# Kernel optimization log

Measured on AMD Instinct MI355X. Metric: run time of the kernel, lower is better.

## Reference

```python
import jax, jax.numpy as jnp
import numpy as np

B, CIN, COUT, H, W = 4, 128, 128, 128, 128
K, G, PAD = 3, 4, 1  # kernel_size, deformable_groups, padding=(K-1)//2
CG = CIN // G


def setup_inputs() -> dict:
    key = jax.random.key(0)
    k1, k2, k3, k4 = jax.random.split(key, 4)
    x = jax.random.normal(k1, (B, CIN, H, W), jnp.float32)
    # 1x1 offset conv (in module it is zero-initialized; use small random values
    # so the bilinear-sampling path is actually exercised)
    w_off = jax.random.normal(k2, (G * K * K * 2, CIN), jnp.float32) * 0.01
    b_off = jax.random.normal(k3, (G * K * K * 2,), jnp.float32) * 0.1
    # DeformConv weight [Cout, Cin, K, K] (DCNv1 has no bias)
    w_def = jax.random.normal(k4, (COUT, CIN, K, K), jnp.float32) * (1.0 / np.sqrt(CIN * K * K))
    return {"x": x, "w_off": w_off, "b_off": b_off, "w_def": w_def}


def _deform_conv(x, offset, w):
    """DCNv1: per-location bilinear gather at offset positions, then weighted sum.

    x:      [B, CIN, H, W]
    offset: [B, G*K*K*2, H, W], channel layout (g, kk, {dy,dx})
    w:      [COUT, CIN, K, K]
    """
    off = offset.reshape(B, G, K * K, 2, H, W)
    ky, kx = np.meshgrid(np.arange(K), np.arange(K), indexing='ij')
    ky = jnp.asarray(ky.reshape(-1), jnp.float32)
    kx = jnp.asarray(kx.reshape(-1), jnp.float32)
    # sampling positions: p = p0 + p_k - pad + offset   -> [B, G, K*K, H, W]
    py = off[:, :, :, 0] + (ky - PAD).reshape(1, 1, K * K, 1, 1) \
         + jnp.arange(H, dtype=jnp.float32).reshape(1, 1, 1, H, 1)
    px = off[:, :, :, 1] + (kx - PAD).reshape(1, 1, K * K, 1, 1) \
         + jnp.arange(W, dtype=jnp.float32).reshape(1, 1, 1, 1, W)

    y0 = jnp.floor(py)
    x0 = jnp.floor(px)
    wy1 = py - y0
    wx1 = px - x0
    wy0 = 1.0 - wy1
    wx0 = 1.0 - wx1
    y0i = y0.astype(jnp.int32)
    x0i = x0.astype(jnp.int32)

    xg = x.reshape(B, G, CG, H * W)  # grouped channels for gather

    def gather(yi, xi):
        # zero padding outside the feature map (mmcv DeformConv semantics)
        valid = (yi >= 0) & (yi < H) & (xi >= 0) & (xi < W)
        idx = (jnp.clip(yi, 0, H - 1) * W + jnp.clip(xi, 0, W - 1)).reshape(B, G, 1, K * K * H * W)
        v = jnp.take_along_axis(xg, idx, axis=3).reshape(B, G, CG, K * K, H, W)
        return v * valid[:, :, None].astype(x.dtype)

    # accumulate the four bilinear corners sequentially to bound peak memory
    val = gather(y0i, x0i) * (wy0 * wx0)[:, :, None]
    val = val + gather(y0i, x0i + 1) * (wy0 * wx1)[:, :, None]
    val = val + gather(y0i + 1, x0i) * (wy1 * wx0)[:, :, None]
    val = val + gather(y0i + 1, x0i + 1) * (wy1 * wx1)[:, :, None]

    wg = w.reshape(COUT, G, CG, K * K)
    return jnp.einsum('bgckhw,ogck->bohw', val, wg)


def reference(x, w_off, b_off, w_def):
    # 1x1 offset conv with bias
    offset = jnp.einsum('bchw,oc->bohw', x, w_off) + b_off[None, :, None, None]
    return jax.nn.relu(_deform_conv(x, offset, w_def))
```

## Files before the change

kernel.cpp:

```cpp
#include <hip/hip_runtime.h>
#include <hip/hip_fp16.h>


#define HW 16384

typedef _Float16 h2 __attribute__((ext_vector_type(2)));
typedef _Float16 h8 __attribute__((ext_vector_type(8)));
typedef float floatx4 __attribute__((ext_vector_type(4)));

static __device__ __forceinline__ unsigned pkrtz(float a, float b) {
  auto h = __builtin_amdgcn_cvt_pkrtz(a, b);
  return __builtin_bit_cast(unsigned, h);
}
static __device__ __forceinline__ h2 u2h2(unsigned u) { return __builtin_bit_cast(h2, u); }
static __device__ __forceinline__ unsigned h2u(h2 h) { return __builtin_bit_cast(unsigned, h); }
static __device__ __forceinline__ h2 splat_lo(unsigned u) {
  unsigned v = (u & 0xffffu) | (u << 16); return u2h2(v);
}
static __device__ __forceinline__ h2 splat_hi(unsigned u) {
  unsigned v = (u >> 16) | (u & 0xffff0000u); return u2h2(v);
}

__global__ __launch_bounds__(256) void prep_w(
    const float* __restrict__ w_off, const float* __restrict__ w_def,
    _Float16* __restrict__ woff, _Float16* __restrict__ wdef) {
  int idx = blockIdx.x * 256 + threadIdx.x;
  int stride = gridDim.x * 256;
  for (int i = idx; i < 147456; i += stride) {
    int j = i & 7, l = (i >> 3) & 63, ot = (i >> 9) & 7, ks = (i >> 12) & 3, kk = i >> 14;
    int o = ot * 16 + (l & 15);
    int c = ks * 32 + ((l >> 4) << 3) + j;
    wdef[i] = (_Float16)w_def[(o * 128 + c) * 9 + kk];
  }
  for (int i = idx; i < 10240; i += stride) {
    int j = i & 7, l = (i >> 3) & 63, t = i >> 9;
    int mt = t % 5, ks = t / 5;
    int o = mt * 16 + (l & 15);
    int c = ks * 32 + ((l >> 4) << 3) + j;
    woff[i] = (o < 72) ? (_Float16)w_off[o * 128 + c] : (_Float16)0.f;
  }
}

__global__ __launch_bounds__(256) void prep_row(
    const float* __restrict__ x, const _Float16* __restrict__ woff,
    const float* __restrict__ b_off, unsigned* __restrict__ offs2,
    _Float16* __restrict__ x16) {
  __shared__ uint2 xpk[32 * 64];
  int tid = threadIdx.x, lane = tid & 63, wv = tid >> 6;
  int i = blockIdx.x;
  int L = (i & 7) * 128 + (i >> 3);
  int half = L & 1, h = (L >> 1) & 127, b = L >> 8;
  int p0 = half * 64;

#pragma unroll
  for (int it = 0; it < 2; it++) {
    int u = it * 256 + tid;
    int px4 = u & 15, cqq = u >> 4;
    const float* xp = x + (((size_t)b * 128 + cqq * 4) * 128 + h) * 128 + p0 + px4 * 4;
    float4 v0 = *(const float4*)xp;
    float4 v1 = *(const float4*)(xp + HW);
    float4 v2 = *(const float4*)(xp + 2 * HW);
    float4 v3 = *(const float4*)(xp + 3 * HW);
    uint2* dst = &xpk[cqq * 64 + px4 * 4];
    uint2 w;
    w.x = pkrtz(v0.x, v1.x); w.y = pkrtz(v2.x, v3.x); dst[0] = w;
    w.x = pkrtz(v0.y, v1.y); w.y = pkrtz(v2.y, v3.y); dst[1] = w;
    w.x = pkrtz(v0.z, v1.z); w.y = pkrtz(v2.z, v3.z); dst[2] = w;
    w.x = pkrtz(v0.w, v1.w); w.y = pkrtz(v2.w, v3.w); dst[3] = w;
  }
  __syncthreads();

  uint4* xrow = (uint4*)(x16 + (((size_t)b * 128 + h) * 128 + p0) * 128);
#pragma unroll
  for (int it = 0; it < 4; it++) {
    int u = it * 256 + tid;
    int oct = u & 15, px = u >> 4;
    uint2 a = xpk[(2 * oct) * 64 + px];
    uint2 c = xpk[(2 * oct + 1) * 64 + px];
    uint4 qv; qv.x = a.x; qv.y = a.y; qv.z = c.x; qv.w = c.y;
    xrow[px * 16 + oct] = qv;
  }

  floatx4 acc[5];
#pragma unroll
  for (int mt = 0; mt < 5; mt++) acc[mt] = (floatx4)0.f;
  const h8* A = (const h8*)woff;
  int q = lane >> 4, col = lane & 15;
  int pxl = wv * 16 + col;
#pragma unroll
  for (int ks = 0; ks < 4; ks++) {
    uint2 lo = xpk[(ks * 8 + 2 * q) * 64 + pxl];
    uint2 hi = xpk[(ks * 8 + 2 * q + 1) * 64 + pxl];
    uint4 qq; qq.x = lo.x; qq.y = lo.y; qq.z = hi.x; qq.w = hi.y;
    h8 bv = __builtin_bit_cast(h8, qq);
#pragma unroll
    for (int mt = 0; mt < 5; mt++)
      acc[mt] = __builtin_amdgcn_mfma_f32_16x16x32_f16(A[(ks * 5 + mt) * 64 + lane], bv, acc[mt], 0, 0, 0);
  }
#pragma unroll
  for (int mt = 0; mt < 5; mt++) {
    if (mt == 4 && q >= 2) continue;
    int o0 = mt * 16 + q * 4;
    float4 bo = *(const float4*)(b_off + o0);
    floatx4 f = acc[mt];
    unsigned* dst = offs2 + ((size_t)b * 36 + (o0 >> 1)) * HW + h * 128 + p0 + pxl;
    dst[0]  = pkrtz(f[0] + bo.x, f[1] + bo.y);
    dst[HW] = pkrtz(f[2] + bo.z, f[3] + bo.w);
  }
}

__global__ __launch_bounds__(256, 3) void deform_conv(
    const _Float16* __restrict__ x16, const _Float16* __restrict__ wdef,
    const unsigned* __restrict__ offs2, float* __restrict__ out) {
  __shared__ uint4 xs[5 * 128 * 5];

  int tid = threadIdx.x, lane = tid & 63, wv = tid >> 6;
  int i = blockIdx.x;
  int L = (i & 7) * 64 + (i >> 3);
  int b = L >> 7, h = L & 127;
  int rlo = min(max(h - 2, 0), 123);
  int pa = 32 * wv + (lane & 15);
  int q = lane >> 4;

  floatx4 acc[2][8];
#pragma unroll
  for (int f = 0; f < 2; f++)
#pragma unroll
    for (int ot = 0; ot < 8; ot++) acc[f][ot] = (floatx4)0.f;

  for (int t = 0; t < 4; t++) {
    __syncthreads();
    unsigned dd[9][2];
#pragma unroll
    for (int kk = 0; kk < 9; kk++)
#pragma unroll
      for (int f = 0; f < 2; f++)
        dd[kk][f] = offs2[((size_t)b * 36 + t * 9 + kk) * HW + h * 128 + pa + 16 * f];
#pragma unroll
    for (int it = 0; it < 10; it++) {
      int u = tid + it * 256;
      int oct = u & 3, v2 = u >> 2;
      int px = v2 & 127, r = v2 >> 7;
      const uint4* src = (const uint4*)(x16 + (((size_t)b * 128 + rlo + r) * 128 + px) * 128 + t * 32) + oct;
      xs[(r * 128 + px) * 5 + oct] = *src;
    }
    __syncthreads();

#pragma unroll
    for (int kk = 0; kk < 9; kk++) {
      const uint4* Ak = (const uint4*)wdef + (size_t)(kk * 2048 + t * 512);
      h8 av[8];
#pragma unroll
      for (int ot = 0; ot < 8; ot++) av[ot] = __builtin_bit_cast(h8, Ak[ot * 64 + lane]);
#pragma unroll
      for (int f = 0; f < 2; f++) {
        int p = pa + 16 * f;
        h2 d = u2h2(dd[kk][f]);
        float dy = (float)d[0], dx = (float)d[1];
        float py = (float)h + (float)(kk / 3 - 1) + dy;
        float pxs = (float)p + (float)(kk % 3 - 1) + dx;
        float y0f = floorf(py), x0f = floorf(pxs);
        int y0 = (int)y0f, x0 = (int)x0f;
        float wy1f = py - y0f, wx1 = pxs - x0f;
        float wy0f = 1.f - wy1f, wx0 = 1.f - wx1;
        int x1 = x0 + 1, y1 = y0 + 1;
        int xb = min(max(x0, 0), 126);
        float fx0 = (x0 >= 0 && x0 <= 127) ? 1.f : 0.f;
        float fx1 = (x1 >= 0 && x1 <= 127) ? 1.f : 0.f;
        float wAf = (x0 == xb ? wx0 * fx0 : 0.f) + (x1 == xb ? wx1 * fx1 : 0.f);
        float wBf = (x0 == xb + 1 ? wx0 * fx0 : 0.f) + (x1 == xb + 1 ? wx1 * fx1 : 0.f);
        float fy0 = (y0 >= 0 && y0 <= 127) ? 1.f : 0.f;
        float fy1 = (y1 >= 0 && y1 <= 127) ? 1.f : 0.f;
        int r0 = min(max(min(max(y0, 0), 127) - rlo, 0), 4);
        int r1 = min(max(min(max(y1, 0), 127) - rlo, 0), 4);
        float wy0e = wy0f * fy0, wy1e = wy1f * fy1;
        unsigned w0_pk = pkrtz(wy0e * wAf, wy0e * wBf);
        unsigned w1_pk = pkrtz(wy1e * wAf, wy1e * wBf);

        int i0 = (r0 * 128 + xb) * 5 + q;
        int i1 = (r1 * 128 + xb) * 5 + q;
        uint4 P = xs[i0], Q = xs[i0 + 5], R = xs[i1], S = xs[i1 + 5];
        h2 w00 = splat_lo(w0_pk), w01 = splat_hi(w0_pk);
        h2 w10 = splat_lo(w1_pk), w11 = splat_hi(w1_pk);
        uint4 bq;
        bq.x = h2u(w00 * u2h2(P.x) + w01 * u2h2(Q.x) + w10 * u2h2(R.x) + w11 * u2h2(S.x));
        bq.y = h2u(w00 * u2h2(P.y) + w01 * u2h2(Q.y) + w10 * u2h2(R.y) + w11 * u2h2(S.y));
        bq.z = h2u(w00 * u2h2(P.z) + w01 * u2h2(Q.z) + w10 * u2h2(R.z) + w11 * u2h2(S.z));
        bq.w = h2u(w00 * u2h2(P.w) + w01 * u2h2(Q.w) + w10 * u2h2(R.w) + w11 * u2h2(S.w));
        h8 bv = __builtin_bit_cast(h8, bq);
#pragma unroll
        for (int ot = 0; ot < 8; ot++)
          acc[f][ot] = __builtin_amdgcn_mfma_f32_16x16x32_f16(av[ot], bv, acc[f][ot], 0, 0, 0);
      }
    }
  }

#pragma unroll
  for (int f = 0; f < 2; f++) {
    float* ob = out + (size_t)b * 128 * HW + h * 128 + pa + 16 * f;
#pragma unroll
    for (int ot = 0; ot < 8; ot++) {
      floatx4 fv = acc[f][ot];
#pragma unroll
      for (int reg = 0; reg < 4; reg++) {
        int o = ot * 16 + q * 4 + reg;
        ob[(size_t)o * HW] = fmaxf(fv[reg], 0.f);
      }
    }
  }
}

extern "C" void kernel_launch(void* const* d_in, const int* in_sizes, int n_in,
                              void* d_out, int out_size, void* d_ws, size_t ws_size,
                              hipStream_t stream) {
  const float* x     = (const float*)d_in[0];
  const float* w_off = (const float*)d_in[1];
  const float* b_off = (const float*)d_in[2];
  const float* w_def = (const float*)d_in[3];
  float* out = (float*)d_out;

  _Float16* wdef = (_Float16*)d_ws;
  _Float16* woff = (_Float16*)((char*)d_ws + 294912);
  unsigned* offs2 = (unsigned*)((char*)d_ws + 315392);
  _Float16* x16  = (_Float16*)((char*)d_ws + 9752576);

  prep_w<<<dim3(288), dim3(256), 0, stream>>>(w_off, w_def, woff, wdef);
  prep_row<<<dim3(1024), dim3(256), 0, stream>>>(x, woff, b_off, offs2, x16);
  deform_conv<<<dim3(512), dim3(256), 0, stream>>>(x16, wdef, offs2, out);
}
```

Before: 153.3 us.

## Precompute bilinear weights and indices once per pixel into shared memory

Each pixel's bilinear weights and gather indices used to be computed redundantly by all four lane quads (q) that share a pixel column. Now the 288 records per wave (9 taps x 32 pixels) are computed once, spread across lanes, stored to shared memory, and read back in the MFMA loop. This removes 4x redundant ALU work and the offset register array. The price is extra LDS traffic and a lower occupancy hint (launch bounds 3 to 2 waves), which may reduce latency hiding.

```diff
diff --git a/kernel.cpp b/kernel.cpp
--- a/kernel.cpp
+++ b/kernel.cpp
@@ -109,18 +109,20 @@
   }
 }
 
-__global__ __launch_bounds__(256, 3) void deform_conv(
+__global__ __launch_bounds__(256, 2) void deform_conv(
     const _Float16* __restrict__ x16, const _Float16* __restrict__ wdef,
     const unsigned* __restrict__ offs2, float* __restrict__ out) {
   __shared__ uint4 xs[5 * 128 * 5];
+  __shared__ uint2 rec_w[4][9][32];
+  __shared__ unsigned rec_i[4][9][32];
 
   int tid = threadIdx.x, lane = tid & 63, wv = tid >> 6;
   int i = blockIdx.x;
   int L = (i & 7) * 64 + (i >> 3);
   int b = L >> 7, h = L & 127;
   int rlo = min(max(h - 2, 0), 123);
-  int pa = 32 * wv + (lane & 15);
   int q = lane >> 4;
+  int col = lane & 15;
 
   floatx4 acc[2][8];
 #pragma unroll
@@ -130,32 +132,14 @@
 
   for (int t = 0; t < 4; t++) {
     __syncthreads();
-    unsigned dd[9][2];
-#pragma unroll
-    for (int kk = 0; kk < 9; kk++)
-#pragma unroll
-      for (int f = 0; f < 2; f++)
-        dd[kk][f] = offs2[((size_t)b * 36 + t * 9 + kk) * HW + h * 128 + pa + 16 * f];
-#pragma unroll
-    for (int it = 0; it < 10; it++) {
-      int u = tid + it * 256;
-      int oct = u & 3, v2 = u >> 2;
-      int px = v2 & 127, r = v2 >> 7;
-      const uint4* src = (const uint4*)(x16 + (((size_t)b * 128 + rlo + r) * 128 + px) * 128 + t * 32) + oct;
-      xs[(r * 128 + px) * 5 + oct] = *src;
-    }
-    __syncthreads();
-
-#pragma unroll
-    for (int kk = 0; kk < 9; kk++) {
-      const uint4* Ak = (const uint4*)wdef + (size_t)(kk * 2048 + t * 512);
-      h8 av[8];
-#pragma unroll
-      for (int ot = 0; ot < 8; ot++) av[ot] = __builtin_bit_cast(h8, Ak[ot * 64 + lane]);
-#pragma unroll
-      for (int f = 0; f < 2; f++) {
-        int p = pa + 16 * f;
-        h2 d = u2h2(dd[kk][f]);
+#pragma unroll
+    for (int it = 0; it < 5; it++) {
+      int u = it * 64 + lane;
+      if (u < 288) {
+        int kk = u >> 5, pl = u & 31;
+        int p = 32 * wv + pl;
+        unsigned dd = offs2[((size_t)b * 36 + t * 9 + kk) * HW + h * 128 + p];
+        h2 d = u2h2(dd);
         float dy = (float)d[0], dx = (float)d[1];
         float py = (float)h + (float)(kk / 3 - 1) + dy;
         float pxs = (float)p + (float)(kk % 3 - 1) + dx;
@@ -174,14 +158,41 @@
         int r0 = min(max(min(max(y0, 0), 127) - rlo, 0), 4);
         int r1 = min(max(min(max(y1, 0), 127) - rlo, 0), 4);
         float wy0e = wy0f * fy0, wy1e = wy1f * fy1;
-        unsigned w0_pk = pkrtz(wy0e * wAf, wy0e * wBf);
-        unsigned w1_pk = pkrtz(wy1e * wAf, wy1e * wBf);
-
-        int i0 = (r0 * 128 + xb) * 5 + q;
-        int i1 = (r1 * 128 + xb) * 5 + q;
+        uint2 rw;
+        rw.x = pkrtz(wy0e * wAf, wy0e * wBf);
+        rw.y = pkrtz(wy1e * wAf, wy1e * wBf);
+        rec_w[wv][kk][pl] = rw;
+        unsigned i0 = (unsigned)((r0 * 128 + xb) * 5);
+        unsigned i1 = (unsigned)((r1 * 128 + xb) * 5);
+        rec_i[wv][kk][pl] = i0 | (i1 << 16);
+      }
+    }
+#pragma unroll
+    for (int it = 0; it < 10; it++) {
+      int u = tid + it * 256;
+      int oct = u & 3, v2 = u >> 2;
+      int px = v2 & 127, r = v2 >> 7;
+      const uint4* src = (const uint4*)(x16 + (((size_t)b * 128 + rlo + r) * 128 + px) * 128 + t * 32) + oct;
+      xs[(r * 128 + px) * 5 + oct] = *src;
+    }
+    __syncthreads();
+
+#pragma unroll
+    for (int kk = 0; kk < 9; kk++) {
+      const uint4* Ak = (const uint4*)wdef + (size_t)(kk * 2048 + t * 512);
+      h8 av[8];
+#pragma unroll
+      for (int ot = 0; ot < 8; ot++) av[ot] = __builtin_bit_cast(h8, Ak[ot * 64 + lane]);
+#pragma unroll
+      for (int f = 0; f < 2; f++) {
+        int sl = 16 * f + col;
+        uint2 rw = rec_w[wv][kk][sl];
+        unsigned ii = rec_i[wv][kk][sl];
+        int i0 = (int)(ii & 0xffffu) + q;
+        int i1 = (int)(ii >> 16) + q;
         uint4 P = xs[i0], Q = xs[i0 + 5], R = xs[i1], S = xs[i1 + 5];
-        h2 w00 = splat_lo(w0_pk), w01 = splat_hi(w0_pk);
-        h2 w10 = splat_lo(w1_pk), w11 = splat_hi(w1_pk);
+        h2 w00 = splat_lo(rw.x), w01 = splat_hi(rw.x);
+        h2 w10 = splat_lo(rw.y), w11 = splat_hi(rw.y);
         uint4 bq;
         bq.x = h2u(w00 * u2h2(P.x) + w01 * u2h2(Q.x) + w10 * u2h2(R.x) + w11 * u2h2(S.x));
         bq.y = h2u(w00 * u2h2(P.y) + w01 * u2h2(Q.y) + w10 * u2h2(R.y) + w11 * u2h2(S.y));
@@ -197,7 +208,7 @@
 
 #pragma unroll
   for (int f = 0; f < 2; f++) {
-    float* ob = out + (size_t)b * 128 * HW + h * 128 + pa + 16 * f;
+    float* ob = out + (size_t)b * 128 * HW + h * 128 + 32 * wv + col + 16 * f;
 #pragma unroll
     for (int ot = 0; ot < 8; ot++) {
       floatx4 fv = acc[f][ot];
```

After: 131.2 us. 14.4% less time.
